# Performance work log

Hardware: AMD Instinct MI355X
Metric: run time of the kernel (lower is better)

The kernel has to match this reference:

```python
import jax, jax.numpy as jnp
import numpy as np

VOCAB = 128
HID = 1024
STD = 0.01


def setup_inputs() -> dict:
    key = jax.random.key(0)
    ks = jax.random.split(key, 9)
    X = jax.random.randint(ks[0], (64, 512), 0, VOCAB, dtype=jnp.int32)
    def w(k, shape):
        return jax.random.normal(k, shape, dtype=jnp.float32) * STD
    return {
        "X": X,
        # reset gate
        "Wr_x": w(ks[1], (VOCAB, HID)), "Wr_h": w(ks[2], (HID, HID)), "b_r": jnp.zeros(HID, jnp.float32),
        # update gate
        "Wz_x": w(ks[3], (VOCAB, HID)), "Wz_h": w(ks[4], (HID, HID)), "b_z": jnp.zeros(HID, jnp.float32),
        # candidate
        "Wh_x": w(ks[5], (VOCAB, HID)), "Wh_h": w(ks[6], (HID, HID)), "b_h": jnp.zeros(HID, jnp.float32),
        # output head
        "W_o": w(ks[7], (HID, VOCAB)), "b_o": jnp.zeros(VOCAB, jnp.float32),
    }


def reference(X, Wr_x, Wr_h, b_r, Wz_x, Wz_h, b_z, Wh_x, Wh_h, b_h, W_o, b_o):
    B, T = X.shape
    # one-hot encode all timesteps: (T, B, V)
    Xoh = jax.nn.one_hot(X.T, VOCAB, dtype=jnp.float32)

    def step(h, x_t):
        # x_t: (B, V), h: (B, H)
        r = jax.nn.sigmoid(x_t @ Wr_x + h @ Wr_h + b_r)
        z = jax.nn.sigmoid(x_t @ Wz_x + h @ Wz_h + b_z)
        h_tilde = jnp.tanh(x_t @ Wh_x + (r * h) @ Wh_h + b_h)
        h_new = z * h + (1.0 - z) * h_tilde
        out = h_new @ W_o + b_o  # (B, V)
        return h_new, out

    h0 = jnp.zeros((B, HID), jnp.float32)
    _, outs = jax.lax.scan(step, h0, Xoh)  # outs: (T, B, V)
    return jnp.transpose(outs, (1, 0, 2))  # (B, T, V)
```

## Files before the change

### kernel.cpp

```cpp
#include <hip/hip_runtime.h>

#define HID   1024
#define TLEN  512
#define VOC   128
#define NBLK  256
#define NW    32
#define NO    2
#define LDSK  1032
#define HBUF  (64 * HID)
#define OD    16

typedef __bf16 bf16_t;
typedef __attribute__((ext_vector_type(8))) __bf16 bf16x8;
typedef __attribute__((ext_vector_type(4))) float  f32x4;
typedef __attribute__((ext_vector_type(2))) float  f32x2;
typedef __attribute__((ext_vector_type(4))) unsigned uint4v;

__device__ __forceinline__ float sigmoid_fast(float x) {
  return 1.0f / (1.0f + __expf(-x));
}
__device__ __forceinline__ float tanh_fast(float x) {
  float e = __expf(-2.0f * x);
  return (1.0f - e) / (1.0f + e);
}

union PairU { bf16_t b[2]; unsigned u; };

__device__ __forceinline__ void l1_inv() {
  asm volatile("buffer_inv" ::: "memory");
}

__device__ __forceinline__ void st_sc1(bf16_t* p, float f0, float f1) {
  PairU c; c.b[0] = (bf16_t)f0; c.b[1] = (bf16_t)f1;
  __hip_atomic_store((unsigned*)p, c.u, __ATOMIC_RELAXED, __HIP_MEMORY_SCOPE_AGENT);
}
__device__ __forceinline__ bf16x8 ld_nt16(const bf16_t* p) {
  union { uint4v u; bf16x8 b; } c;
  c.u = __builtin_nontemporal_load((const uint4v*)p);
  return c.b;
}

__device__ __forceinline__ void wait1(const unsigned* ctr, unsigned tgt) {
  if (threadIdx.x == 0) {
    while (__hip_atomic_load(ctr, __ATOMIC_RELAXED, __HIP_MEMORY_SCOPE_AGENT) < tgt)
      __builtin_amdgcn_s_sleep(1);
  }
  __syncthreads();
}

__device__ __forceinline__ void wait_rh_oc(const unsigned* rctr, const unsigned* oc0,
                                           const unsigned* oc1, unsigned tgt, unsigned otgt) {
  if (threadIdx.x < 64) {
    const int lane = threadIdx.x;
    for (;;) {
      bool ok = true;
      if (lane == 0)      ok = __hip_atomic_load(rctr, __ATOMIC_RELAXED, __HIP_MEMORY_SCOPE_AGENT) >= tgt;
      else if (lane == 1) ok = __hip_atomic_load(oc0,  __ATOMIC_RELAXED, __HIP_MEMORY_SCOPE_AGENT) >= otgt;
      else if (lane == 2) ok = __hip_atomic_load(oc1,  __ATOMIC_RELAXED, __HIP_MEMORY_SCOPE_AGENT) >= otgt;
      if (__all(ok)) break;
      __builtin_amdgcn_s_sleep(1);
    }
  }
  __syncthreads();
}

__device__ __forceinline__ void publish_add(unsigned* ctr) {
  __syncthreads();
  if (threadIdx.x == 0)
    __hip_atomic_fetch_add(ctr, 1u, __ATOMIC_RELAXED, __HIP_MEMORY_SCOPE_AGENT);
}
__device__ __forceinline__ void publish_val(unsigned* f, unsigned v) {
  __syncthreads();
  if (threadIdx.x == 0)
    __hip_atomic_store(f, v, __ATOMIC_RELAXED, __HIP_MEMORY_SCOPE_AGENT);
}

#define MFMA(a, b, c) __builtin_amdgcn_mfma_f32_16x16x32_bf16((a), (b), (c), 0, 0, 0)

__global__ void __launch_bounds__(256, 1)
gru_ctr(const int* __restrict__ X,
        const float* __restrict__ Wr_x, const float* __restrict__ Wr_h, const float* __restrict__ b_r,
        const float* __restrict__ Wz_x, const float* __restrict__ Wz_h, const float* __restrict__ b_z,
        const float* __restrict__ Wh_x, const float* __restrict__ Wh_h, const float* __restrict__ b_h,
        const float* __restrict__ W_o,  const float* __restrict__ b_o,
        float* __restrict__ out,
        bf16_t* __restrict__ hring, bf16_t* __restrict__ rh_bf,
        bf16_t* __restrict__ oring, bf16_t* __restrict__ wz_bf,
        unsigned* __restrict__ flags)
{
  __shared__ __align__(16) bf16_t Wbuf[2 * 32 * LDSK];
  __shared__ int s_role;

  unsigned* h_ctr  = flags;
  unsigned* rh_ctr = flags + 32;
  unsigned* oc0    = flags + 64;
  unsigned* oc1    = flags + 96;
  unsigned* cnt    = flags + 128;
  unsigned* winner = flags + 160;
  unsigned* ocnt   = flags + 164;

  const int tid  = threadIdx.x;
  const int lane = tid & 63;
  const int wv   = tid >> 6;
  const int n16  = lane & 15;
  const int q    = lane >> 4;
  const int aoff = (wv * 16 + n16) * HID + q * 8;

  int bi[4];
#pragma unroll
  for (int i = 0; i < 4; ++i) bi[i] = wv * 16 + q * 4 + i;

  if (tid == 0) {
    unsigned xcc;
    asm volatile("s_getreg_b32 %0, hwreg(HW_REG_XCC_ID)" : "=s"(xcc));
    xcc &= 7u;
    unsigned idx = __hip_atomic_fetch_add(&cnt[xcc], 1u, __ATOMIC_RELAXED, __HIP_MEMORY_SCOPE_AGENT);
    if (idx == NW - 1) {
      unsigned exp = 0u;
      __hip_atomic_compare_exchange_strong(winner, &exp, xcc + 1u,
          __ATOMIC_RELAXED, __ATOMIC_RELAXED, __HIP_MEMORY_SCOPE_AGENT);
    }
    unsigned w;
    do {
      w = __hip_atomic_load(winner, __ATOMIC_RELAXED, __HIP_MEMORY_SCOPE_AGENT);
      __builtin_amdgcn_s_sleep(1);
    } while (w == 0u);
    if (xcc == w - 1u && idx < NW) {
      s_role = (int)idx;
    } else {
      unsigned o = __hip_atomic_fetch_add(ocnt, 1u, __ATOMIC_RELAXED, __HIP_MEMORY_SCOPE_AGENT);
      s_role = (o < NO) ? (NW + (int)o) : -1;
    }
  }
  __syncthreads();
  const int role = s_role;
  if (role < 0) return;

  if (role < NW) {
    const int s  = role;
    const int c0 = s * 32;
    for (int idx = tid; idx < 32 * HID; idx += 256) {
      int n = idx & 31, k = idx >> 5;
      int r = (n & 1) * 16 + (n >> 1);
      Wbuf[r * LDSK + k]             = (bf16_t)Wr_h[k * HID + c0 + n];
      Wbuf[32 * LDSK + r * LDSK + k] = (bf16_t)Wh_h[k * HID + c0 + n];
    }
    bf16_t* wzs = wz_bf + s * (32 * 1024);
    for (int idx = tid; idx < 32 * HID; idx += 256) {
      int n = idx & 31, k = idx >> 5;
      int r = (n & 1) * 16 + (n >> 1);
      wzs[r * 1024 + k] = (bf16_t)Wz_h[k * HID + c0 + n];
    }

    const int j0 = c0 + 2 * n16;
#pragma unroll
    for (int i = 0; i < 4; ++i) {
      PairU zz; zz.b[0] = (bf16_t)0.f; zz.b[1] = (bf16_t)0.f;
      *reinterpret_cast<PairU*>(hring + bi[i] * HID + j0) = zz;
    }
    publish_add(h_ctr);

    const float br0 = b_r[j0], br1 = b_r[j0 + 1];
    const float bz0 = b_z[j0], bz1 = b_z[j0 + 1];
    const float bh0 = b_h[j0], bh1 = b_h[j0 + 1];
    const bf16_t* wr0 = &Wbuf[n16 * LDSK + q * 8];
    const bf16_t* wr1 = &Wbuf[(16 + n16) * LDSK + q * 8];
    const bf16_t* wh0 = &Wbuf[32 * LDSK + n16 * LDSK + q * 8];
    const bf16_t* wh1 = &Wbuf[32 * LDSK + (16 + n16) * LDSK + q * 8];
    const bf16_t* wz0 = wzs + n16 * 1024 + q * 8;
    const bf16_t* wz1 = wzs + (16 + n16) * 1024 + q * 8;
    const bf16_t* rhrow = rh_bf + aoff;

    f32x4 hm0 = {0.f,0.f,0.f,0.f}, hm1 = {0.f,0.f,0.f,0.f};

    for (int t = 0; t < TLEN; ++t) {
      float gr0[4], gr1[4], gz0[4], gz1[4], gh0[4], gh1[4];
#pragma unroll
      for (int i = 0; i < 4; ++i) {
        int xb = X[bi[i] * TLEN + t];
        gr0[i] = Wr_x[xb * HID + j0]; gr1[i] = Wr_x[xb * HID + j0 + 1];
        gz0[i] = Wz_x[xb * HID + j0]; gz1[i] = Wz_x[xb * HID + j0 + 1];
        gh0[i] = Wh_x[xb * HID + j0]; gh1[i] = Wh_x[xb * HID + j0 + 1];
      }
      wait1(h_ctr, (unsigned)(NW * (t + 1)));
      l1_inv();
      const bf16_t* hslot = hring + (t & 1) * HBUF;
      const bf16_t* hrow  = hslot + aoff;
      bf16x8 areg[32];
#pragma unroll
      for (int kk = 0; kk < 32; ++kk)
        areg[kk] = *reinterpret_cast<const bf16x8*>(hrow + kk * 32);
      f32x4 aR0 = {0.f,0.f,0.f,0.f}, aR1 = {0.f,0.f,0.f,0.f};
#pragma unroll
      for (int kk = 0; kk < 32; ++kk) {
        bf16x8 w0 = *reinterpret_cast<const bf16x8*>(wr0 + kk * 32);
        bf16x8 w1 = *reinterpret_cast<const bf16x8*>(wr1 + kk * 32);
        aR0 = MFMA(areg[kk], w0, aR0);
        aR1 = MFMA(areg[kk], w1, aR1);
      }
#pragma unroll
      for (int i = 0; i < 4; ++i) {
        float r0 = sigmoid_fast(aR0[i] + br0 + gr0[i]);
        float r1 = sigmoid_fast(aR1[i] + br1 + gr1[i]);
        PairU hp = *reinterpret_cast<const PairU*>(hslot + bi[i] * HID + j0);
        PairU c;
        c.b[0] = (bf16_t)(r0 * (float)hp.b[0]);
        c.b[1] = (bf16_t)(r1 * (float)hp.b[1]);
        *reinterpret_cast<PairU*>(rh_bf + bi[i] * HID + j0) = c;
      }
      publish_add(rh_ctr);

      f32x4 aZ0 = {0.f,0.f,0.f,0.f}, aZ1 = {0.f,0.f,0.f,0.f};
#pragma unroll
      for (int kk = 0; kk < 32; ++kk) {
        bf16x8 w0 = *reinterpret_cast<const bf16x8*>(wz0 + kk * 32);
        bf16x8 w1 = *reinterpret_cast<const bf16x8*>(wz1 + kk * 32);
        aZ0 = MFMA(areg[kk], w0, aZ0);
        aZ1 = MFMA(areg[kk], w1, aZ1);
      }
      f32x4 z0, z1;
#pragma unroll
      for (int i = 0; i < 4; ++i) {
        z0[i] = sigmoid_fast(aZ0[i] + bz0 + gz0[i]);
        z1[i] = sigmoid_fast(aZ1[i] + bz1 + gz1[i]);
      }

      unsigned otgt = (t > OD - 1) ? (unsigned)(t + 1 - OD) : 0u;
      wait_rh_oc(rh_ctr, oc0, oc1, (unsigned)(NW * (t + 1)), otgt);
      l1_inv();
      bf16x8 breg[32];
#pragma unroll
      for (int kk = 0; kk < 32; ++kk)
        breg[kk] = *reinterpret_cast<const bf16x8*>(rhrow + kk * 32);
      f32x4 aH0 = {0.f,0.f,0.f,0.f}, aH1 = {0.f,0.f,0.f,0.f};
#pragma unroll
      for (int kk = 0; kk < 32; ++kk) {
        bf16x8 w0 = *reinterpret_cast<const bf16x8*>(wh0 + kk * 32);
        bf16x8 w1 = *reinterpret_cast<const bf16x8*>(wh1 + kk * 32);
        aH0 = MFMA(breg[kk], w0, aH0);
        aH1 = MFMA(breg[kk], w1, aH1);
      }
      bf16_t* hnext = hring + ((t + 1) & 1) * HBUF;
      bf16_t* onext = oring + ((t + 1) % OD) * HBUF;
#pragma unroll
      for (int i = 0; i < 4; ++i) {
        float ht0 = tanh_fast(aH0[i] + bh0 + gh0[i]);
        float ht1 = tanh_fast(aH1[i] + bh1 + gh1[i]);
        float hn0 = z0[i] * hm0[i] + (1.f - z0[i]) * ht0;
        float hn1 = z1[i] * hm1[i] + (1.f - z1[i]) * ht1;
        hm0[i] = hn0; hm1[i] = hn1;
        PairU c; c.b[0] = (bf16_t)hn0; c.b[1] = (bf16_t)hn1;
        *reinterpret_cast<PairU*>(hnext + bi[i] * HID + j0) = c;
        st_sc1(onext + bi[i] * HID + j0, hn0, hn1);
      }
      publish_add(h_ctr);
    }
    __builtin_amdgcn_fence(__ATOMIC_RELEASE, "agent");
  } else {
    const int ob  = role - NW;
    const int c0o = ob * 64;
    for (int idx = tid; idx < 64 * HID; idx += 256) {
      int n = idx & 63, k = idx >> 6;
      int g = n >> 5, m = n & 31;
      int r = g * 32 + (m & 1) * 16 + (m >> 1);
      Wbuf[r * LDSK + k] = (bf16_t)W_o[k * VOC + c0o + n];
    }
    __syncthreads();

    float bo[2][2];
#pragma unroll
    for (int g = 0; g < 2; ++g) {
      bo[g][0] = b_o[c0o + 32 * g + 2 * n16];
      bo[g][1] = b_o[c0o + 32 * g + 2 * n16 + 1];
    }
    const bf16_t* wo[2][2];
#pragma unroll
    for (int g = 0; g < 2; ++g)
#pragma unroll
      for (int h = 0; h < 2; ++h)
        wo[g][h] = &Wbuf[(g * 32 + h * 16 + n16) * LDSK + q * 8];

    unsigned* myoc = (ob == 0) ? oc0 : oc1;
    for (int t = 1; t <= TLEN; ++t) {
      wait1(h_ctr, (unsigned)(NW * (t + 1)));
      const bf16_t* hrow = oring + (t % OD) * HBUF + aoff;
      bf16x8 areg[32];
#pragma unroll
      for (int kk = 0; kk < 32; ++kk)
        areg[kk] = ld_nt16(hrow + kk * 32);
      f32x4 acc[2][2];
#pragma unroll
      for (int g = 0; g < 2; ++g)
#pragma unroll
        for (int h = 0; h < 2; ++h)
          acc[g][h] = (f32x4){0.f, 0.f, 0.f, 0.f};
#pragma unroll
      for (int kk = 0; kk < 32; ++kk) {
#pragma unroll
        for (int g = 0; g < 2; ++g) {
          bf16x8 w0 = *reinterpret_cast<const bf16x8*>(wo[g][0] + kk * 32);
          bf16x8 w1 = *reinterpret_cast<const bf16x8*>(wo[g][1] + kk * 32);
          acc[g][0] = MFMA(areg[kk], w0, acc[g][0]);
          acc[g][1] = MFMA(areg[kk], w1, acc[g][1]);
        }
      }
#pragma unroll
      for (int g = 0; g < 2; ++g) {
        const int j0 = c0o + 32 * g + 2 * n16;
#pragma unroll
        for (int i = 0; i < 4; ++i) {
          f32x2 v = {acc[g][0][i] + bo[g][0], acc[g][1][i] + bo[g][1]};
          *reinterpret_cast<f32x2*>(&out[(bi[i] * TLEN + (t - 1)) * VOC + j0]) = v;
        }
      }
      publish_val(myoc, (unsigned)t);
    }
  }
}

extern "C" void kernel_launch(void* const* d_in, const int* in_sizes, int n_in,
                              void* d_out, int out_size, void* d_ws, size_t ws_size,
                              hipStream_t stream) {
  const int*   X    = (const int*)d_in[0];
  const float* Wr_x = (const float*)d_in[1];
  const float* Wr_h = (const float*)d_in[2];
  const float* b_r  = (const float*)d_in[3];
  const float* Wz_x = (const float*)d_in[4];
  const float* Wz_h = (const float*)d_in[5];
  const float* b_z  = (const float*)d_in[6];
  const float* Wh_x = (const float*)d_in[7];
  const float* Wh_h = (const float*)d_in[8];
  const float* b_h  = (const float*)d_in[9];
  const float* W_o  = (const float*)d_in[10];
  const float* b_o  = (const float*)d_in[11];

  char* ws = (char*)d_ws;
  unsigned* flags = (unsigned*)ws;
  bf16_t*   hring = (bf16_t*)(ws + 4096);
  bf16_t*   rh_bf = (bf16_t*)(ws + 4096 + 2 * HBUF * sizeof(bf16_t));
  bf16_t*   oring = (bf16_t*)(ws + 4096 + 3 * HBUF * sizeof(bf16_t));
  bf16_t*   wz_bf = (bf16_t*)(ws + 4096 + (3 + OD) * HBUF * sizeof(bf16_t));

  hipMemsetAsync(ws, 0, 4096, stream);

  gru_ctr<<<NBLK, 256, 0, stream>>>(
      X, Wr_x, Wr_h, b_r, Wz_x, Wz_h, b_z, Wh_x, Wh_h, b_h, W_o, b_o,
      (float*)d_out, hring, rh_bf, oring, wz_bf, flags);
}
```

Baseline: 8.454 ms.

## Fold output head into worker blocks and replace counters with per-block flags

Removes the two dedicated output-head blocks and their ring buffer, and has each of the 32 worker blocks compute a 16-column slice of the output projection from the h tile it already holds in registers. The shared atomic-add counters become per-block flag arrays, polled by a 32-lane wave with __all, so a publish is a plain store rather than a contended atomic. The MFMA chains are split into two independent accumulators to shorten dependency latency. The r*h product now uses the fp32 hidden state kept in registers instead of reloading bf16 h. In exchange, one wave per block does extra MFMA work on the critical path each step, and there is an added start-up barrier plus a final output step after the loop.

```diff
diff --git a/kernel.cpp b/kernel.cpp
--- a/kernel.cpp
+++ b/kernel.cpp
@@ -5,16 +5,12 @@
 #define VOC   128
 #define NBLK  256
 #define NW    32
-#define NO    2
 #define LDSK  1032
 #define HBUF  (64 * HID)
-#define OD    16
 
 typedef __bf16 bf16_t;
 typedef __attribute__((ext_vector_type(8))) __bf16 bf16x8;
 typedef __attribute__((ext_vector_type(4))) float  f32x4;
-typedef __attribute__((ext_vector_type(2))) float  f32x2;
-typedef __attribute__((ext_vector_type(4))) unsigned uint4v;
 
 __device__ __forceinline__ float sigmoid_fast(float x) {
   return 1.0f / (1.0f + __expf(-x));
@@ -30,74 +26,50 @@
   asm volatile("buffer_inv" ::: "memory");
 }
 
-__device__ __forceinline__ void st_sc1(bf16_t* p, float f0, float f1) {
-  PairU c; c.b[0] = (bf16_t)f0; c.b[1] = (bf16_t)f1;
-  __hip_atomic_store((unsigned*)p, c.u, __ATOMIC_RELAXED, __HIP_MEMORY_SCOPE_AGENT);
-}
-__device__ __forceinline__ bf16x8 ld_nt16(const bf16_t* p) {
-  union { uint4v u; bf16x8 b; } c;
-  c.u = __builtin_nontemporal_load((const uint4v*)p);
-  return c.b;
-}
-
-__device__ __forceinline__ void wait1(const unsigned* ctr, unsigned tgt) {
-  if (threadIdx.x == 0) {
-    while (__hip_atomic_load(ctr, __ATOMIC_RELAXED, __HIP_MEMORY_SCOPE_AGENT) < tgt)
+__device__ __forceinline__ bf16x8 ldw(const bf16_t* p) {
+  return *reinterpret_cast<const bf16x8*>(p);
+}
+
+__device__ __forceinline__ void wait_flags(const unsigned* f, unsigned tgt) {
+  if (threadIdx.x < 64) {
+    const volatile unsigned* p =
+        (const volatile unsigned*)(f + (threadIdx.x & 31));
+    for (;;) {
+      l1_inv();
+      unsigned v = *p;
+      if (__all((int)(v - tgt) >= 0)) break;
       __builtin_amdgcn_s_sleep(1);
-  }
-  __syncthreads();
-}
-
-__device__ __forceinline__ void wait_rh_oc(const unsigned* rctr, const unsigned* oc0,
-                                           const unsigned* oc1, unsigned tgt, unsigned otgt) {
-  if (threadIdx.x < 64) {
-    const int lane = threadIdx.x;
-    for (;;) {
-      bool ok = true;
-      if (lane == 0)      ok = __hip_atomic_load(rctr, __ATOMIC_RELAXED, __HIP_MEMORY_SCOPE_AGENT) >= tgt;
-      else if (lane == 1) ok = __hip_atomic_load(oc0,  __ATOMIC_RELAXED, __HIP_MEMORY_SCOPE_AGENT) >= otgt;
-      else if (lane == 2) ok = __hip_atomic_load(oc1,  __ATOMIC_RELAXED, __HIP_MEMORY_SCOPE_AGENT) >= otgt;
-      if (__all(ok)) break;
-      __builtin_amdgcn_s_sleep(1);
-    }
-  }
-  __syncthreads();
-}
-
-__device__ __forceinline__ void publish_add(unsigned* ctr) {
-  __syncthreads();
-  if (threadIdx.x == 0)
-    __hip_atomic_fetch_add(ctr, 1u, __ATOMIC_RELAXED, __HIP_MEMORY_SCOPE_AGENT);
-}
-__device__ __forceinline__ void publish_val(unsigned* f, unsigned v) {
-  __syncthreads();
-  if (threadIdx.x == 0)
-    __hip_atomic_store(f, v, __ATOMIC_RELAXED, __HIP_MEMORY_SCOPE_AGENT);
+    }
+  }
+  __syncthreads();
+}
+
+__device__ __forceinline__ void publish(unsigned* fw, unsigned v) {
+  __syncthreads();
+  if (threadIdx.x == 0) *(volatile unsigned*)fw = v;
 }
 
 #define MFMA(a, b, c) __builtin_amdgcn_mfma_f32_16x16x32_bf16((a), (b), (c), 0, 0, 0)
 
 __global__ void __launch_bounds__(256, 1)
-gru_ctr(const int* __restrict__ X,
-        const float* __restrict__ Wr_x, const float* __restrict__ Wr_h, const float* __restrict__ b_r,
-        const float* __restrict__ Wz_x, const float* __restrict__ Wz_h, const float* __restrict__ b_z,
-        const float* __restrict__ Wh_x, const float* __restrict__ Wh_h, const float* __restrict__ b_h,
-        const float* __restrict__ W_o,  const float* __restrict__ b_o,
-        float* __restrict__ out,
-        bf16_t* __restrict__ hring, bf16_t* __restrict__ rh_bf,
-        bf16_t* __restrict__ oring, bf16_t* __restrict__ wz_bf,
-        unsigned* __restrict__ flags)
+gru_team(const int* __restrict__ X,
+         const float* __restrict__ Wr_x, const float* __restrict__ Wr_h, const float* __restrict__ b_r,
+         const float* __restrict__ Wz_x, const float* __restrict__ Wz_h, const float* __restrict__ b_z,
+         const float* __restrict__ Wh_x, const float* __restrict__ Wh_h, const float* __restrict__ b_h,
+         const float* __restrict__ W_o,  const float* __restrict__ b_o,
+         float* __restrict__ out,
+         bf16_t* __restrict__ hring, bf16_t* __restrict__ rh_bf,
+         bf16_t* __restrict__ wz_bf, bf16_t* __restrict__ wo_bf,
+         unsigned* __restrict__ flags)
 {
   __shared__ __align__(16) bf16_t Wbuf[2 * 32 * LDSK];
   __shared__ int s_role;
 
-  unsigned* h_ctr  = flags;
-  unsigned* rh_ctr = flags + 32;
-  unsigned* oc0    = flags + 64;
-  unsigned* oc1    = flags + 96;
+  unsigned* fH     = flags;
+  unsigned* fR     = flags + 32;
   unsigned* cnt    = flags + 128;
   unsigned* winner = flags + 160;
-  unsigned* ocnt   = flags + 164;
+  unsigned* ready  = flags + 168;
 
   const int tid  = threadIdx.x;
   const int lane = tid & 63;
@@ -125,197 +97,190 @@
       w = __hip_atomic_load(winner, __ATOMIC_RELAXED, __HIP_MEMORY_SCOPE_AGENT);
       __builtin_amdgcn_s_sleep(1);
     } while (w == 0u);
-    if (xcc == w - 1u && idx < NW) {
-      s_role = (int)idx;
-    } else {
-      unsigned o = __hip_atomic_fetch_add(ocnt, 1u, __ATOMIC_RELAXED, __HIP_MEMORY_SCOPE_AGENT);
-      s_role = (o < NO) ? (NW + (int)o) : -1;
-    }
+    s_role = (xcc == w - 1u && idx < NW) ? (int)idx : -1;
   }
   __syncthreads();
   const int role = s_role;
   if (role < 0) return;
 
-  if (role < NW) {
-    const int s  = role;
-    const int c0 = s * 32;
-    for (int idx = tid; idx < 32 * HID; idx += 256) {
-      int n = idx & 31, k = idx >> 5;
-      int r = (n & 1) * 16 + (n >> 1);
-      Wbuf[r * LDSK + k]             = (bf16_t)Wr_h[k * HID + c0 + n];
-      Wbuf[32 * LDSK + r * LDSK + k] = (bf16_t)Wh_h[k * HID + c0 + n];
-    }
-    bf16_t* wzs = wz_bf + s * (32 * 1024);
-    for (int idx = tid; idx < 32 * HID; idx += 256) {
-      int n = idx & 31, k = idx >> 5;
-      int r = (n & 1) * 16 + (n >> 1);
-      wzs[r * 1024 + k] = (bf16_t)Wz_h[k * HID + c0 + n];
-    }
-
-    const int j0 = c0 + 2 * n16;
+  const int s  = role;
+  const int c0 = s * 32;
+
+  if (tid == 0) {
+    *(volatile unsigned*)&fH[s] = 0u;
+    *(volatile unsigned*)&fR[s] = 0u;
+  }
+
+  for (int idx = tid; idx < 32 * HID; idx += 256) {
+    int n = idx & 31, k = idx >> 5;
+    int r = (n & 1) * 16 + (n >> 1);
+    Wbuf[r * LDSK + k]             = (bf16_t)Wr_h[k * HID + c0 + n];
+    Wbuf[32 * LDSK + r * LDSK + k] = (bf16_t)Wh_h[k * HID + c0 + n];
+  }
+  bf16_t* wzs = wz_bf + s * (32 * 1024);
+  for (int idx = tid; idx < 32 * HID; idx += 256) {
+    int n = idx & 31, k = idx >> 5;
+    int r = (n & 1) * 16 + (n >> 1);
+    wzs[r * 1024 + k] = (bf16_t)Wz_h[k * HID + c0 + n];
+  }
+  if (s < 8) {
+    bf16_t* wos = wo_bf + s * (16 * 1024);
+    for (int idx = tid; idx < 16 * HID; idx += 256) {
+      int n = idx & 15, k = idx >> 4;
+      wos[n * 1024 + k] = (bf16_t)W_o[k * VOC + s * 16 + n];
+    }
+  }
+  const int j0 = c0 + 2 * n16;
+#pragma unroll
+  for (int i = 0; i < 4; ++i) {
+    PairU zz; zz.b[0] = (bf16_t)0.f; zz.b[1] = (bf16_t)0.f;
+    *reinterpret_cast<PairU*>(hring + bi[i] * HID + j0) = zz;
+  }
+  __syncthreads();
+
+  if (tid == 0) {
+    __hip_atomic_fetch_add(ready, 1u, __ATOMIC_RELAXED, __HIP_MEMORY_SCOPE_AGENT);
+    while (__hip_atomic_load(ready, __ATOMIC_RELAXED, __HIP_MEMORY_SCOPE_AGENT) < NW)
+      __builtin_amdgcn_s_sleep(1);
+  }
+  __syncthreads();
+  if (tid == 0) *(volatile unsigned*)&fH[s] = 1u;
+
+  const float br0 = b_r[j0], br1 = b_r[j0 + 1];
+  const float bz0 = b_z[j0], bz1 = b_z[j0 + 1];
+  const float bh0 = b_h[j0], bh1 = b_h[j0 + 1];
+  const bf16_t* wr0 = &Wbuf[n16 * LDSK + q * 8];
+  const bf16_t* wr1 = &Wbuf[(16 + n16) * LDSK + q * 8];
+  const bf16_t* wh0 = &Wbuf[32 * LDSK + n16 * LDSK + q * 8];
+  const bf16_t* wh1 = &Wbuf[32 * LDSK + (16 + n16) * LDSK + q * 8];
+  const bf16_t* wz0 = wzs + n16 * 1024 + q * 8;
+  const bf16_t* wz1 = wzs + (16 + n16) * 1024 + q * 8;
+  const bf16_t* rhrow = rh_bf + aoff;
+
+  const int rt = s >> 3, vt = s & 7;
+  const bool outw = (wv == rt);
+  const bf16_t* wop = wo_bf + vt * (16 * 1024) + n16 * 1024 + q * 8;
+  const float bo = b_o[vt * 16 + n16];
+
+  f32x4 hm0 = {0.f,0.f,0.f,0.f}, hm1 = {0.f,0.f,0.f,0.f};
+
+  for (int t = 0; t < TLEN; ++t) {
+    float gr0[4], gr1[4], gz0[4], gz1[4], gh0[4], gh1[4];
 #pragma unroll
     for (int i = 0; i < 4; ++i) {
-      PairU zz; zz.b[0] = (bf16_t)0.f; zz.b[1] = (bf16_t)0.f;
-      *reinterpret_cast<PairU*>(hring + bi[i] * HID + j0) = zz;
-    }
-    publish_add(h_ctr);
-
-    const float br0 = b_r[j0], br1 = b_r[j0 + 1];
-    const float bz0 = b_z[j0], bz1 = b_z[j0 + 1];
-    const float bh0 = b_h[j0], bh1 = b_h[j0 + 1];
-    const bf16_t* wr0 = &Wbuf[n16 * LDSK + q * 8];
-    const bf16_t* wr1 = &Wbuf[(16 + n16) * LDSK + q * 8];
-    const bf16_t* wh0 = &Wbuf[32 * LDSK + n16 * LDSK + q * 8];
-    const bf16_t* wh1 = &Wbuf[32 * LDSK + (16 + n16) * LDSK + q * 8];
-    const bf16_t* wz0 = wzs + n16 * 1024 + q * 8;
-    const bf16_t* wz1 = wzs + (16 + n16) * 1024 + q * 8;
-    const bf16_t* rhrow = rh_bf + aoff;
-
-    f32x4 hm0 = {0.f,0.f,0.f,0.f}, hm1 = {0.f,0.f,0.f,0.f};
-
-    for (int t = 0; t < TLEN; ++t) {
-      float gr0[4], gr1[4], gz0[4], gz1[4], gh0[4], gh1[4];
-#pragma unroll
-      for (int i = 0; i < 4; ++i) {
-        int xb = X[bi[i] * TLEN + t];
-        gr0[i] = Wr_x[xb * HID + j0]; gr1[i] = Wr_x[xb * HID + j0 + 1];
-        gz0[i] = Wz_x[xb * HID + j0]; gz1[i] = Wz_x[xb * HID + j0 + 1];
-        gh0[i] = Wh_x[xb * HID + j0]; gh1[i] = Wh_x[xb * HID + j0 + 1];
+      int xb = X[bi[i] * TLEN + t];
+      gr0[i] = Wr_x[xb * HID + j0]; gr1[i] = Wr_x[xb * HID + j0 + 1];
+      gz0[i] = Wz_x[xb * HID + j0]; gz1[i] = Wz_x[xb * HID + j0 + 1];
+      gh0[i] = Wh_x[xb * HID + j0]; gh1[i] = Wh_x[xb * HID + j0 + 1];
+    }
+
+    wait_flags(fH, (unsigned)(t + 1));
+    l1_inv();
+    const bf16_t* hrow = hring + (t & 1) * HBUF + aoff;
+    bf16x8 areg[32];
+#pragma unroll
+    for (int kk = 0; kk < 32; ++kk) areg[kk] = ldw(hrow + kk * 32);
+
+    f32x4 aR0 = {0.f,0.f,0.f,0.f}, aR1 = {0.f,0.f,0.f,0.f};
+    f32x4 bR0 = {0.f,0.f,0.f,0.f}, bR1 = {0.f,0.f,0.f,0.f};
+#pragma unroll
+    for (int kk = 0; kk < 16; ++kk) {
+      aR0 = MFMA(areg[kk],      ldw(wr0 + kk * 32),        aR0);
+      aR1 = MFMA(areg[kk],      ldw(wr1 + kk * 32),        aR1);
+      bR0 = MFMA(areg[kk + 16], ldw(wr0 + (kk + 16) * 32), bR0);
+      bR1 = MFMA(areg[kk + 16], ldw(wr1 + (kk + 16) * 32), bR1);
+    }
+    aR0 += bR0; aR1 += bR1;
+#pragma unroll
+    for (int i = 0; i < 4; ++i) {
+      float r0 = sigmoid_fast(aR0[i] + br0 + gr0[i]);
+      float r1 = sigmoid_fast(aR1[i] + br1 + gr1[i]);
+      PairU c;
+      c.b[0] = (bf16_t)(r0 * hm0[i]);
+      c.b[1] = (bf16_t)(r1 * hm1[i]);
+      *reinterpret_cast<PairU*>(rh_bf + bi[i] * HID + j0) = c;
+    }
+    publish(&fR[s], (unsigned)(t + 1));
+
+    if (outw && t) {
+      f32x4 oa = {0.f,0.f,0.f,0.f}, ob = {0.f,0.f,0.f,0.f};
+#pragma unroll
+      for (int kk = 0; kk < 16; ++kk) {
+        oa = MFMA(areg[kk],      ldw(wop + kk * 32),        oa);
+        ob = MFMA(areg[kk + 16], ldw(wop + (kk + 16) * 32), ob);
       }
-      wait1(h_ctr, (unsigned)(NW * (t + 1)));
-      l1_inv();
-      const bf16_t* hslot = hring + (t & 1) * HBUF;
-      const bf16_t* hrow  = hslot + aoff;
-      bf16x8 areg[32];
-#pragma unroll
-      for (int kk = 0; kk < 32; ++kk)
-        areg[kk] = *reinterpret_cast<const bf16x8*>(hrow + kk * 32);
-      f32x4 aR0 = {0.f,0.f,0.f,0.f}, aR1 = {0.f,0.f,0.f,0.f};
-#pragma unroll
-      for (int kk = 0; kk < 32; ++kk) {
-        bf16x8 w0 = *reinterpret_cast<const bf16x8*>(wr0 + kk * 32);
-        bf16x8 w1 = *reinterpret_cast<const bf16x8*>(wr1 + kk * 32);
-        aR0 = MFMA(areg[kk], w0, aR0);
-        aR1 = MFMA(areg[kk], w1, aR1);
-      }
-#pragma unroll
-      for (int i = 0; i < 4; ++i) {
-        float r0 = sigmoid_fast(aR0[i] + br0 + gr0[i]);
-        float r1 = sigmoid_fast(aR1[i] + br1 + gr1[i]);
-        PairU hp = *reinterpret_cast<const PairU*>(hslot + bi[i] * HID + j0);
-        PairU c;
-        c.b[0] = (bf16_t)(r0 * (float)hp.b[0]);
-        c.b[1] = (bf16_t)(r1 * (float)hp.b[1]);
-        *reinterpret_cast<PairU*>(rh_bf + bi[i] * HID + j0) = c;
-      }
-      publish_add(rh_ctr);
-
-      f32x4 aZ0 = {0.f,0.f,0.f,0.f}, aZ1 = {0.f,0.f,0.f,0.f};
-#pragma unroll
-      for (int kk = 0; kk < 32; ++kk) {
-        bf16x8 w0 = *reinterpret_cast<const bf16x8*>(wz0 + kk * 32);
-        bf16x8 w1 = *reinterpret_cast<const bf16x8*>(wz1 + kk * 32);
-        aZ0 = MFMA(areg[kk], w0, aZ0);
-        aZ1 = MFMA(areg[kk], w1, aZ1);
-      }
-      f32x4 z0, z1;
-#pragma unroll
-      for (int i = 0; i < 4; ++i) {
-        z0[i] = sigmoid_fast(aZ0[i] + bz0 + gz0[i]);
-        z1[i] = sigmoid_fast(aZ1[i] + bz1 + gz1[i]);
-      }
-
-      unsigned otgt = (t > OD - 1) ? (unsigned)(t + 1 - OD) : 0u;
-      wait_rh_oc(rh_ctr, oc0, oc1, (unsigned)(NW * (t + 1)), otgt);
-      l1_inv();
-      bf16x8 breg[32];
-#pragma unroll
-      for (int kk = 0; kk < 32; ++kk)
-        breg[kk] = *reinterpret_cast<const bf16x8*>(rhrow + kk * 32);
-      f32x4 aH0 = {0.f,0.f,0.f,0.f}, aH1 = {0.f,0.f,0.f,0.f};
-#pragma unroll
-      for (int kk = 0; kk < 32; ++kk) {
-        bf16x8 w0 = *reinterpret_cast<const bf16x8*>(wh0 + kk * 32);
-        bf16x8 w1 = *reinterpret_cast<const bf16x8*>(wh1 + kk * 32);
-        aH0 = MFMA(breg[kk], w0, aH0);
-        aH1 = MFMA(breg[kk], w1, aH1);
-      }
-      bf16_t* hnext = hring + ((t + 1) & 1) * HBUF;
-      bf16_t* onext = oring + ((t + 1) % OD) * HBUF;
-#pragma unroll
-      for (int i = 0; i < 4; ++i) {
-        float ht0 = tanh_fast(aH0[i] + bh0 + gh0[i]);
-        float ht1 = tanh_fast(aH1[i] + bh1 + gh1[i]);
-        float hn0 = z0[i] * hm0[i] + (1.f - z0[i]) * ht0;
-        float hn1 = z1[i] * hm1[i] + (1.f - z1[i]) * ht1;
-        hm0[i] = hn0; hm1[i] = hn1;
-        PairU c; c.b[0] = (bf16_t)hn0; c.b[1] = (bf16_t)hn1;
-        *reinterpret_cast<PairU*>(hnext + bi[i] * HID + j0) = c;
-        st_sc1(onext + bi[i] * HID + j0, hn0, hn1);
-      }
-      publish_add(h_ctr);
-    }
-    __builtin_amdgcn_fence(__ATOMIC_RELEASE, "agent");
-  } else {
-    const int ob  = role - NW;
-    const int c0o = ob * 64;
-    for (int idx = tid; idx < 64 * HID; idx += 256) {
-      int n = idx & 63, k = idx >> 6;
-      int g = n >> 5, m = n & 31;
-      int r = g * 32 + (m & 1) * 16 + (m >> 1);
-      Wbuf[r * LDSK + k] = (bf16_t)W_o[k * VOC + c0o + n];
-    }
-    __syncthreads();
-
-    float bo[2][2];
-#pragma unroll
-    for (int g = 0; g < 2; ++g) {
-      bo[g][0] = b_o[c0o + 32 * g + 2 * n16];
-      bo[g][1] = b_o[c0o + 32 * g + 2 * n16 + 1];
-    }
-    const bf16_t* wo[2][2];
-#pragma unroll
-    for (int g = 0; g < 2; ++g)
-#pragma unroll
-      for (int h = 0; h < 2; ++h)
-        wo[g][h] = &Wbuf[(g * 32 + h * 16 + n16) * LDSK + q * 8];
-
-    unsigned* myoc = (ob == 0) ? oc0 : oc1;
-    for (int t = 1; t <= TLEN; ++t) {
-      wait1(h_ctr, (unsigned)(NW * (t + 1)));
-      const bf16_t* hrow = oring + (t % OD) * HBUF + aoff;
-      bf16x8 areg[32];
-#pragma unroll
-      for (int kk = 0; kk < 32; ++kk)
-        areg[kk] = ld_nt16(hrow + kk * 32);
-      f32x4 acc[2][2];
-#pragma unroll
-      for (int g = 0; g < 2; ++g)
-#pragma unroll
-        for (int h = 0; h < 2; ++h)
-          acc[g][h] = (f32x4){0.f, 0.f, 0.f, 0.f};
-#pragma unroll
-      for (int kk = 0; kk < 32; ++kk) {
-#pragma unroll
-        for (int g = 0; g < 2; ++g) {
-          bf16x8 w0 = *reinterpret_cast<const bf16x8*>(wo[g][0] + kk * 32);
-          bf16x8 w1 = *reinterpret_cast<const bf16x8*>(wo[g][1] + kk * 32);
-          acc[g][0] = MFMA(areg[kk], w0, acc[g][0]);
-          acc[g][1] = MFMA(areg[kk], w1, acc[g][1]);
-        }
-      }
-#pragma unroll
-      for (int g = 0; g < 2; ++g) {
-        const int j0 = c0o + 32 * g + 2 * n16;
-#pragma unroll
-        for (int i = 0; i < 4; ++i) {
-          f32x2 v = {acc[g][0][i] + bo[g][0], acc[g][1][i] + bo[g][1]};
-          *reinterpret_cast<f32x2*>(&out[(bi[i] * TLEN + (t - 1)) * VOC + j0]) = v;
-        }
-      }
-      publish_val(myoc, (unsigned)t);
-    }
-  }
+      oa += ob;
+#pragma unroll
+      for (int i = 0; i < 4; ++i)
+        out[(bi[i] * TLEN + (t - 1)) * VOC + vt * 16 + n16] = oa[i] + bo;
+    }
+
+    f32x4 aZ0 = {0.f,0.f,0.f,0.f}, aZ1 = {0.f,0.f,0.f,0.f};
+    f32x4 bZ0 = {0.f,0.f,0.f,0.f}, bZ1 = {0.f,0.f,0.f,0.f};
+#pragma unroll
+    for (int kk = 0; kk < 16; ++kk) {
+      aZ0 = MFMA(areg[kk],      ldw(wz0 + kk * 32),        aZ0);
+      aZ1 = MFMA(areg[kk],      ldw(wz1 + kk * 32),        aZ1);
+      bZ0 = MFMA(areg[kk + 16], ldw(wz0 + (kk + 16) * 32), bZ0);
+      bZ1 = MFMA(areg[kk + 16], ldw(wz1 + (kk + 16) * 32), bZ1);
+    }
+    aZ0 += bZ0; aZ1 += bZ1;
+    f32x4 z0, z1;
+#pragma unroll
+    for (int i = 0; i < 4; ++i) {
+      z0[i] = sigmoid_fast(aZ0[i] + bz0 + gz0[i]);
+      z1[i] = sigmoid_fast(aZ1[i] + bz1 + gz1[i]);
+    }
+
+    wait_flags(fR, (unsigned)(t + 1));
+    l1_inv();
+    bf16x8 breg[32];
+#pragma unroll
+    for (int kk = 0; kk < 32; ++kk) breg[kk] = ldw(rhrow + kk * 32);
+    f32x4 aH0 = {0.f,0.f,0.f,0.f}, aH1 = {0.f,0.f,0.f,0.f};
+    f32x4 bH0 = {0.f,0.f,0.f,0.f}, bH1 = {0.f,0.f,0.f,0.f};
+#pragma unroll
+    for (int kk = 0; kk < 16; ++kk) {
+      aH0 = MFMA(breg[kk],      ldw(wh0 + kk * 32),        aH0);
+      aH1 = MFMA(breg[kk],      ldw(wh1 + kk * 32),        aH1);
+      bH0 = MFMA(breg[kk + 16], ldw(wh0 + (kk + 16) * 32), bH0);
+      bH1 = MFMA(breg[kk + 16], ldw(wh1 + (kk + 16) * 32), bH1);
+    }
+    aH0 += bH0; aH1 += bH1;
+    bf16_t* hnext = hring + ((t + 1) & 1) * HBUF;
+#pragma unroll
+    for (int i = 0; i < 4; ++i) {
+      float ht0 = tanh_fast(aH0[i] + bh0 + gh0[i]);
+      float ht1 = tanh_fast(aH1[i] + bh1 + gh1[i]);
+      float hn0 = z0[i] * hm0[i] + (1.f - z0[i]) * ht0;
+      float hn1 = z1[i] * hm1[i] + (1.f - z1[i]) * ht1;
+      hm0[i] = hn0; hm1[i] = hn1;
+      PairU c; c.b[0] = (bf16_t)hn0; c.b[1] = (bf16_t)hn1;
+      *reinterpret_cast<PairU*>(hnext + bi[i] * HID + j0) = c;
+    }
+    publish(&fH[s], (unsigned)(t + 2));
+  }
+
+  wait_flags(fH, (unsigned)(TLEN + 1));
+  l1_inv();
+  if (outw) {
+    const bf16_t* hrow = hring + (TLEN & 1) * HBUF + aoff;
+    bf16x8 areg[32];
+#pragma unroll
+    for (int kk = 0; kk < 32; ++kk) areg[kk] = ldw(hrow + kk * 32);
+    f32x4 oa = {0.f,0.f,0.f,0.f}, ob = {0.f,0.f,0.f,0.f};
+#pragma unroll
+    for (int kk = 0; kk < 16; ++kk) {
+      oa = MFMA(areg[kk],      ldw(wop + kk * 32),        oa);
+      ob = MFMA(areg[kk + 16], ldw(wop + (kk + 16) * 32), ob);
+    }
+    oa += ob;
+#pragma unroll
+    for (int i = 0; i < 4; ++i)
+      out[(bi[i] * TLEN + (TLEN - 1)) * VOC + vt * 16 + n16] = oa[i] + bo;
+  }
+
+  __builtin_amdgcn_fence(__ATOMIC_RELEASE, "agent");
 }
 
 extern "C" void kernel_launch(void* const* d_in, const int* in_sizes, int n_in,
@@ -338,12 +303,13 @@
   unsigned* flags = (unsigned*)ws;
   bf16_t*   hring = (bf16_t*)(ws + 4096);
   bf16_t*   rh_bf = (bf16_t*)(ws + 4096 + 2 * HBUF * sizeof(bf16_t));
-  bf16_t*   oring = (bf16_t*)(ws + 4096 + 3 * HBUF * sizeof(bf16_t));
-  bf16_t*   wz_bf = (bf16_t*)(ws + 4096 + (3 + OD) * HBUF * sizeof(bf16_t));
+  bf16_t*   wz_bf = (bf16_t*)(ws + 4096 + 3 * HBUF * sizeof(bf16_t));
+  bf16_t*   wo_bf = (bf16_t*)(ws + 4096 + 3 * HBUF * sizeof(bf16_t)
+                              + (size_t)NW * 32 * HID * sizeof(bf16_t));
 
   hipMemsetAsync(ws, 0, 4096, stream);
 
-  gru_ctr<<<NBLK, 256, 0, stream>>>(
+  gru_team<<<NBLK, 256, 0, stream>>>(
       X, Wr_x, Wr_h, b_r, Wz_x, Wz_h, b_z, Wh_x, Wh_h, b_h, W_o, b_o,
-      (float*)d_out, hring, rh_bf, oring, wz_bf, flags);
-}
+      (float*)d_out, hring, rh_bf, wz_bf, wo_bf, flags);
+}
```

Result: slower. 9.291 ms (+9.9%).
